# Optimization experiments

Measured on AMD Instinct MI355X. Metric: run time of the kernel, lower is better.

The kernel has to match this reference:

```python
import jax, jax.numpy as jnp
import numpy as np

ALPHA = 1.5
N_ITER = 50
N_ROWS, N_CLASSES = 4096, 32000


def tsallis_bisect(X, alpha=ALPHA, n_iter=N_ITER):
    """Entmax/Tsallis simplex projection via 50-step bisection (matches
    the standard entmax-bisect forward used by sisl/EvSoftmax)."""
    d = X.shape[-1]
    exp = 1.0 / (alpha - 1.0)          # = 2.0 for alpha = 1.5
    Xs = X * (alpha - 1.0)
    max_val = jnp.max(Xs, axis=-1, keepdims=True)            # [N,1]
    tau_lo = max_val - 1.0
    tau_hi = max_val - (1.0 / d) ** (alpha - 1.0)
    f_lo = jnp.sum(jnp.clip(Xs - tau_lo, 0.0) ** exp, axis=-1, keepdims=True) - 1.0
    dm0 = tau_hi - tau_lo

    def body(carry, _):
        tau_lo, dm, _tau_m = carry
        dm = dm * 0.5
        tau_m = tau_lo + dm                                   # [N,1]
        p_m = jnp.clip(Xs - tau_m, 0.0) ** exp                # [N,d]
        f_m = jnp.sum(p_m, axis=-1, keepdims=True) - 1.0
        mask = (f_m * f_lo) >= 0
        tau_lo = jnp.where(mask, tau_m, tau_lo)
        return (tau_lo, dm, tau_m), None

    (_, _, tau_m), _ = jax.lax.scan(body, (tau_lo, dm0, tau_lo), None, length=n_iter)
    return jnp.clip(Xs - tau_m, 0.0) ** exp                   # final p_m


def setup_inputs() -> dict:
    key = jax.random.key(0)
    X = jax.random.normal(key, (N_ROWS, N_CLASSES), dtype=jnp.float32)
    return {"X": X}


def reference(X):
    p_star = tsallis_bisect(X, ALPHA, N_ITER)
    p_star = p_star / jnp.sum(p_star, axis=1, keepdims=True)
    # safe log: value identical to log(p_star) (log(0) = -inf), but with a
    # well-defined (zero) subgradient at exactly-sparse entries.
    return jnp.where(p_star > 0, jnp.log(jnp.where(p_star > 0, p_star, 1.0)), -jnp.inf)
```

## Files before the change

kernel.cpp:

```cpp
#include <hip/hip_runtime.h>
#include <math.h>


#define NCOLS    32000
#define TPBA     512
#define NFULL    15
#define TAILBASE 30720
#define TAILTHR  320
#define NWAVE    8
#define SEGB     320
#define CAPR     (SEGB * NWAVE)
#define NSLOT    (CAPR / 64)
#define MSEG     512
#define SENT16   ((unsigned short)0xC2C0)
#define CSF      0.0055901699437494742f

__device__ __forceinline__ float wred_max(float x) {
#pragma unroll
  for (int o = 1; o < 64; o <<= 1) x = fmaxf(x, __shfl_xor(x, o, 64));
  return x;
}
__device__ __forceinline__ float wred_addf(float x) {
#pragma unroll
  for (int o = 1; o < 64; o <<= 1) x += __shfl_xor(x, o, 64);
  return x;
}
__device__ __forceinline__ unsigned short to_bf16_safe(float x) {
  unsigned int u = __float_as_uint(x);
  u += 0x7FFFu + ((u >> 16) & 1u);
  unsigned short h = (unsigned short)(u >> 16);
  if ((h & 0x7F80u) == 0x7F80u) h = SENT16;
  return h;
}

__global__ __launch_bounds__(TPBA, 4)
void tsa_stream(const float* __restrict__ X, unsigned short* __restrict__ Out,
                float* __restrict__ tauv, int* __restrict__ cnt,
                float* __restrict__ vals, unsigned short* __restrict__ idxs) {
  __shared__ float s_redf[NWAVE];
  __shared__ int   s_ovf;
  const int t    = threadIdx.x;
  const int lane = t & 63;
  const int wid  = t >> 6;
  const size_t row = blockIdx.x;
  const float* __restrict__ xr      = X + row * (size_t)NCOLS;
  unsigned short* __restrict__ orow = Out + row * (size_t)NCOLS;

  float4 v[16];
#pragma unroll
  for (int j = 0; j < NFULL; ++j)
    v[j] = *reinterpret_cast<const float4*>(xr + j * 2048 + t * 4);
  if (t < TAILTHR)
    v[15] = *reinterpret_cast<const float4*>(xr + TAILBASE + t * 4);
  else
    v[15] = make_float4(-1e30f, -1e30f, -1e30f, -1e30f);

  {
    const unsigned long long SF = 0xC2C0C2C0C2C0C2C0ull;
    unsigned long long* o8 = reinterpret_cast<unsigned long long*>(orow);
#pragma unroll
    for (int i = 0; i < 16; ++i) {
      const int p = t + i * TPBA;
      if (p < NCOLS / 4) __builtin_nontemporal_store(SF, o8 + p);
    }
  }
  if (t == 0) s_ovf = 0;

  float m = -1e30f;
#pragma unroll
  for (int j = 0; j < 16; ++j)
    m = fmaxf(m, fmaxf(fmaxf(v[j].x, v[j].y), fmaxf(v[j].z, v[j].w)));
  m = wred_max(m);
  if (lane == 0) s_redf[wid] = m;
  __syncthreads();
  float mm = s_redf[0];
#pragma unroll
  for (int w = 1; w < NWAVE; ++w) mm = fmaxf(mm, s_redf[w]);
  const float max_val = 0.5f * mm;
  const float tl0 = max_val - 1.0f;
  if (t == 0) tauv[row] = max_val;

  int myc = 0;
#pragma unroll
  for (int j = 0; j < 16; ++j) {
    myc += (v[j].x * 0.5f > tl0) + (v[j].y * 0.5f > tl0) +
           (v[j].z * 0.5f > tl0) + (v[j].w * 0.5f > tl0);
  }
  int pre = myc;
#pragma unroll
  for (int o = 1; o < 64; o <<= 1) {
    int y = __shfl_up(pre, o, 64);
    if (lane >= o) pre += y;
  }
  const int wtot = __shfl(pre, 63, 64);
  if (wtot > SEGB) {
    if (lane == 0) s_ovf = 1;
  } else {
    int wpos = pre - myc;
    float* __restrict__ vb = vals + row * (size_t)CAPR + wid * SEGB;
    unsigned short* __restrict__ ib = idxs + row * (size_t)CAPR + wid * SEGB;
#pragma unroll
    for (int j = 0; j < 16; ++j) {
      const int gidx = (j < NFULL) ? (j * 2048 + t * 4) : (TAILBASE + t * 4);
      float x;
      x = v[j].x * 0.5f; if (x > tl0) { vb[wpos] = x; ib[wpos] = (unsigned short)(gidx + 0); ++wpos; }
      x = v[j].y * 0.5f; if (x > tl0) { vb[wpos] = x; ib[wpos] = (unsigned short)(gidx + 1); ++wpos; }
      x = v[j].z * 0.5f; if (x > tl0) { vb[wpos] = x; ib[wpos] = (unsigned short)(gidx + 2); ++wpos; }
      x = v[j].w * 0.5f; if (x > tl0) { vb[wpos] = x; ib[wpos] = (unsigned short)(gidx + 3); ++wpos; }
    }
    if (lane == 63) cnt[row * NWAVE + wid] = wtot;
  }
  __syncthreads();

  if (s_ovf) {
    if (t == 0) cnt[row * NWAVE] = -1;
    const float th = max_val - CSF;
    auto bsum = [&](float tau) -> float {
      float q = 0.f;
#pragma unroll
      for (int j = 0; j < 16; ++j) {
        float r;
        r = fmaxf(v[j].x * 0.5f - tau, 0.f); q = fmaf(r, r, q);
        r = fmaxf(v[j].y * 0.5f - tau, 0.f); q = fmaf(r, r, q);
        r = fmaxf(v[j].z * 0.5f - tau, 0.f); q = fmaf(r, r, q);
        r = fmaxf(v[j].w * 0.5f - tau, 0.f); q = fmaf(r, r, q);
      }
      q = wred_addf(q);
      if (lane == 0) s_redf[wid] = q;
      __syncthreads();
      float tt = s_redf[0];
#pragma unroll
      for (int w = 1; w < NWAVE; ++w) tt += s_redf[w];
      __syncthreads();
      return tt;
    };
    float tau_lo = tl0, dmv = th - tl0, tau_m = tl0;
    const float f_lo = bsum(tau_lo) - 1.0f;
#pragma unroll 1
    for (int it = 0; it < 50; ++it) {
      dmv *= 0.5f;
      const float tm = tau_lo + dmv;
      if (tm == tau_lo) { tau_m = tau_lo; break; }
      tau_m = tm;
      const float fm = bsum(tm) - 1.0f;
      if (fm * f_lo >= 0.0f) tau_lo = tm;
    }
    const float sf = bsum(tau_m);
#pragma unroll
    for (int j = 0; j < 16; ++j) {
      const bool act = (j < NFULL) || (t < TAILTHR);
      if (act) {
        const int gidx = (j < NFULL) ? (j * 2048 + t * 4) : (TAILBASE + t * 4);
        unsigned short h[4];
        float rc, pn;
        rc = fmaxf(v[j].x * 0.5f - tau_m, 0.f); pn = (rc * rc) / sf; h[0] = (pn > 0.f) ? to_bf16_safe(logf(pn)) : SENT16;
        rc = fmaxf(v[j].y * 0.5f - tau_m, 0.f); pn = (rc * rc) / sf; h[1] = (pn > 0.f) ? to_bf16_safe(logf(pn)) : SENT16;
        rc = fmaxf(v[j].z * 0.5f - tau_m, 0.f); pn = (rc * rc) / sf; h[2] = (pn > 0.f) ? to_bf16_safe(logf(pn)) : SENT16;
        rc = fmaxf(v[j].w * 0.5f - tau_m, 0.f); pn = (rc * rc) / sf; h[3] = (pn > 0.f) ? to_bf16_safe(logf(pn)) : SENT16;
        *reinterpret_cast<uint2*>(orow + gidx) =
            make_uint2((unsigned)h[0] | ((unsigned)h[1] << 16),
                       (unsigned)h[2] | ((unsigned)h[3] << 16));
      }
    }
  }
}

__global__ __launch_bounds__(512, 4)
void tsa_bisect(unsigned short* __restrict__ Out,
                const float* __restrict__ tauv, const int* __restrict__ cnt,
                const float* __restrict__ vals,
                const unsigned short* __restrict__ idxs, int nrows) {
  const int t    = threadIdx.x;
  const int lane = t & 63;
  const int wid  = t >> 6;
  const int row  = blockIdx.x * NWAVE + wid;
  if (row >= nrows) return;

  int c8 = (lane < NWAVE) ? cnt[row * NWAVE + lane] : 0;
  const int c0 = __shfl(c8, 0, 64);
  if (c0 < 0) return;

  const float* __restrict__ vb = vals + (size_t)row * CAPR;

  float cv[NSLOT];
#pragma unroll
  for (int r = 0; r < NSLOT; ++r) cv[r] = vb[lane + r * 64];
#pragma unroll
  for (int r = 0; r < NSLOT; ++r) {
    const int cs = __shfl(c8, r / 5, 64);
    if ((r % 5) * 64 + lane >= cs) cv[r] = -1e30f;
  }

  const float max_val = tauv[row];
  const float tl0 = max_val - 1.0f;
  const float th  = max_val - CSF;

  auto fsum = [&](float tau) -> float {
    float q0 = 0.f, q1 = 0.f, q2 = 0.f, q3 = 0.f;
#pragma unroll
    for (int r = 0; r < NSLOT; r += 4) {
      float a;
      a = fmaxf(cv[r + 0] - tau, 0.f); q0 = fmaf(a, a, q0);
      a = fmaxf(cv[r + 1] - tau, 0.f); q1 = fmaf(a, a, q1);
      a = fmaxf(cv[r + 2] - tau, 0.f); q2 = fmaf(a, a, q2);
      a = fmaxf(cv[r + 3] - tau, 0.f); q3 = fmaf(a, a, q3);
    }
    return wred_addf((q0 + q1) + (q2 + q3));
  };

  float tau_lo = tl0, dmv = th - tl0, tau_m = tl0;
  const float f_lo = fsum(tau_lo) - 1.0f;
#pragma unroll 1
  for (int it = 0; it < 50; ++it) {
    dmv *= 0.5f;
    const float tm = tau_lo + dmv;
    if (tm == tau_lo) { tau_m = tau_lo; break; }
    tau_m = tm;
    const float fm = fsum(tm) - 1.0f;
    if (fm * f_lo >= 0.0f) tau_lo = tm;
  }
  const float sf = fsum(tau_m);

  unsigned short* __restrict__ orow = Out + (size_t)row * NCOLS;
  const unsigned short* __restrict__ ib = idxs + (size_t)row * CAPR;
#pragma unroll 1
  for (int r = 0; r < NSLOT; ++r) {
    const float rc = fmaxf(cv[r] - tau_m, 0.f);
    const float pn = (rc * rc) / sf;
    if (pn > 0.f) orow[ib[lane + r * 64]] = to_bf16_safe(logf(pn));
  }
}

__global__ __launch_bounds__(TPBA, 8)
void tsa_mono(const float* __restrict__ X, unsigned short* __restrict__ Out) {
  __shared__ float          s_redf[NWAVE];
  __shared__ int            s_segk[NWAVE];
  __shared__ int            s_ovf;
  __shared__ float          s_tau, s_sf;
  __shared__ float          s_cand[MSEG * NWAVE];
  __shared__ unsigned short s_cidx[MSEG * NWAVE];

  const int t = threadIdx.x, lane = t & 63, wid = t >> 6;
  const size_t row = blockIdx.x;
  const float* __restrict__ xr      = X + row * (size_t)NCOLS;
  unsigned short* __restrict__ orow = Out + row * (size_t)NCOLS;

  float m = -1e30f;
#pragma unroll 5
  for (int j = 0; j < NFULL; ++j) {
    float4 a = *reinterpret_cast<const float4*>(xr + j * 2048 + t * 4);
    m = fmaxf(m, fmaxf(fmaxf(a.x, a.y), fmaxf(a.z, a.w)));
  }
  if (t < TAILTHR) {
    float4 a = *reinterpret_cast<const float4*>(xr + TAILBASE + t * 4);
    m = fmaxf(m, fmaxf(fmaxf(a.x, a.y), fmaxf(a.z, a.w)));
  }
  m = wred_max(m);
  if (lane == 0) s_redf[wid] = m;
  if (t == 0) s_ovf = 0;
  __syncthreads();
  float mm = s_redf[0];
#pragma unroll
  for (int w = 1; w < NWAVE; ++w) mm = fmaxf(mm, s_redf[w]);
  const float max_val = 0.5f * mm;
  const float tau_lo0 = max_val - 1.0f;
  const float tau_hi  = max_val - CSF;

  {
    int base = 0;
    const int seg0 = wid * MSEG;
    const unsigned long long SFILL = 0xC2C0C2C0C2C0C2C0ull;
#pragma unroll 2
    for (int j = 0; j <= NFULL; ++j) {
      const bool act = (j < NFULL) || (t < TAILTHR);
      const int gidx = (j < NFULL) ? (j * 2048 + t * 4) : (TAILBASE + t * 4);
      float x0 = -1e30f, x1 = -1e30f, x2 = -1e30f, x3 = -1e30f;
      if (act) {
        float4 a = *reinterpret_cast<const float4*>(xr + gidx);
        x0 = a.x * 0.5f; x1 = a.y * 0.5f; x2 = a.z * 0.5f; x3 = a.w * 0.5f;
        __builtin_nontemporal_store(
            SFILL, reinterpret_cast<unsigned long long*>(orow + gidx));
      }
      int c = (x0 > tau_lo0) + (x1 > tau_lo0) + (x2 > tau_lo0) + (x3 > tau_lo0);
      int pre = c;
#pragma unroll
      for (int o = 1; o < 64; o <<= 1) {
        int y = __shfl_up(pre, o, 64);
        if (lane >= o) pre += y;
      }
      const int tot = __shfl(pre, 63, 64);
      if (base + tot <= MSEG) {
        int pos = seg0 + base + (pre - c);
        if (x0 > tau_lo0) { s_cand[pos] = x0; s_cidx[pos] = (unsigned short)(gidx + 0); ++pos; }
        if (x1 > tau_lo0) { s_cand[pos] = x1; s_cidx[pos] = (unsigned short)(gidx + 1); ++pos; }
        if (x2 > tau_lo0) { s_cand[pos] = x2; s_cidx[pos] = (unsigned short)(gidx + 2); ++pos; }
        if (x3 > tau_lo0) { s_cand[pos] = x3; s_cidx[pos] = (unsigned short)(gidx + 3); ++pos; }
      } else if (lane == 0) {
        s_ovf = 1;
      }
      base += tot;
    }
    if (base <= MSEG) {
      const int kp = (base + 63) & ~63;
      for (int i = base + lane; i < kp; i += 64) s_cand[seg0 + i] = -1e30f;
    }
    if (lane == 0) s_segk[wid] = base;
  }
  __syncthreads();

  if (s_ovf == 0) {
    if (wid == 0) {
      int kp[NWAVE];
#pragma unroll
      for (int s = 0; s < NWAVE; ++s) kp[s] = (s_segk[s] + 63) & ~63;
      auto fsum = [&](float tau) -> float {
        float q = 0.f;
#pragma unroll 1
        for (int s = 0; s < NWAVE; ++s) {
          const float* cs = s_cand + s * MSEG;
          const int kps = kp[s];
          for (int i = lane; i < kps; i += 64) {
            const float r = fmaxf(cs[i] - tau, 0.f);
            q = fmaf(r, r, q);
          }
        }
        return wred_addf(q);
      };
      float tau_lo = tau_lo0, dmv = tau_hi - tau_lo0, tau_m = tau_lo0;
      const float f_lo = fsum(tau_lo) - 1.0f;
#pragma unroll 1
      for (int it = 0; it < 50; ++it) {
        dmv *= 0.5f;
        const float tm = tau_lo + dmv;
        if (tm == tau_lo) { tau_m = tau_lo; break; }
        tau_m = tm;
        const float fm = fsum(tm) - 1.0f;
        if (fm * f_lo >= 0.0f) tau_lo = tm;
      }
      const float sf = fsum(tau_m);
      if (lane == 0) { s_tau = tau_m; s_sf = sf; }
    }
    __syncthreads();
    const float tau_m = s_tau, sf = s_sf;
#pragma unroll 1
    for (int s = 0; s < NWAVE; ++s) {
      const int ks = s_segk[s];
      for (int i = t; i < ks; i += TPBA) {
        const float rc = fmaxf(s_cand[s * MSEG + i] - tau_m, 0.f);
        const float pn = (rc * rc) / sf;
        if (pn > 0.f) orow[s_cidx[s * MSEG + i]] = to_bf16_safe(logf(pn));
      }
    }
  } else {
    auto bsum = [&](float tau) -> float {
      float q = 0.f;
#pragma unroll 4
      for (int j = 0; j <= NFULL; ++j) {
        const bool act = (j < NFULL) || (t < TAILTHR);
        const int gidx = (j < NFULL) ? (j * 2048 + t * 4) : (TAILBASE + t * 4);
        if (act) {
          float4 a = *reinterpret_cast<const float4*>(xr + gidx);
          float r;
          r = fmaxf(a.x * 0.5f - tau, 0.f); q = fmaf(r, r, q);
          r = fmaxf(a.y * 0.5f - tau, 0.f); q = fmaf(r, r, q);
          r = fmaxf(a.z * 0.5f - tau, 0.f); q = fmaf(r, r, q);
          r = fmaxf(a.w * 0.5f - tau, 0.f); q = fmaf(r, r, q);
        }
      }
      q = wred_addf(q);
      if (lane == 0) s_redf[wid] = q;
      __syncthreads();
      float tot = s_redf[0];
#pragma unroll
      for (int w = 1; w < NWAVE; ++w) tot += s_redf[w];
      __syncthreads();
      return tot;
    };
    float tau_lo = tau_lo0, dmv = tau_hi - tau_lo0, tau_m = tau_lo0;
    const float f_lo = bsum(tau_lo) - 1.0f;
#pragma unroll 1
    for (int it = 0; it < 50; ++it) {
      dmv *= 0.5f;
      const float tm = tau_lo + dmv;
      if (tm == tau_lo) { tau_m = tau_lo; break; }
      tau_m = tm;
      const float fm = bsum(tm) - 1.0f;
      if (fm * f_lo >= 0.0f) tau_lo = tm;
    }
    const float sf = bsum(tau_m);
#pragma unroll 1
    for (int j = 0; j <= NFULL; ++j) {
      const bool act = (j < NFULL) || (t < TAILTHR);
      const int gidx = (j < NFULL) ? (j * 2048 + t * 4) : (TAILBASE + t * 4);
      if (act) {
        float4 a = *reinterpret_cast<const float4*>(xr + gidx);
        unsigned short h[4];
        float rc, pn;
        rc = fmaxf(a.x * 0.5f - tau_m, 0.f); pn = (rc * rc) / sf; h[0] = (pn > 0.f) ? to_bf16_safe(logf(pn)) : SENT16;
        rc = fmaxf(a.y * 0.5f - tau_m, 0.f); pn = (rc * rc) / sf; h[1] = (pn > 0.f) ? to_bf16_safe(logf(pn)) : SENT16;
        rc = fmaxf(a.z * 0.5f - tau_m, 0.f); pn = (rc * rc) / sf; h[2] = (pn > 0.f) ? to_bf16_safe(logf(pn)) : SENT16;
        rc = fmaxf(a.w * 0.5f - tau_m, 0.f); pn = (rc * rc) / sf; h[3] = (pn > 0.f) ? to_bf16_safe(logf(pn)) : SENT16;
        *reinterpret_cast<uint2*>(orow + gidx) =
            make_uint2((unsigned)h[0] | ((unsigned)h[1] << 16),
                       (unsigned)h[2] | ((unsigned)h[3] << 16));
      }
    }
  }
}

extern "C" void kernel_launch(void* const* d_in, const int* in_sizes, int n_in,
                              void* d_out, int out_size, void* d_ws, size_t ws_size,
                              hipStream_t stream) {
  const float* X = (const float*)d_in[0];
  unsigned short* Out = (unsigned short*)d_out;
  const int rows = in_sizes[0] / NCOLS;

  const size_t offT = 0;
  const size_t offC = (size_t)rows * 4;
  const size_t offV = (offC + (size_t)rows * NWAVE * 4 + 255) & ~(size_t)255;
  const size_t offI = (offV + (size_t)rows * CAPR * 4 + 255) & ~(size_t)255;
  const size_t need = offI + (size_t)rows * CAPR * 2;

  if (ws_size >= need) {
    char* ws = (char*)d_ws;
    float* tauv = (float*)(ws + offT);
    int* cnt = (int*)(ws + offC);
    float* vals = (float*)(ws + offV);
    unsigned short* idxs = (unsigned short*)(ws + offI);
    hipLaunchKernelGGL(tsa_stream, dim3(rows), dim3(TPBA), 0, stream,
                       X, Out, tauv, cnt, vals, idxs);
    const int gridB = (rows + NWAVE - 1) / NWAVE;
    hipLaunchKernelGGL(tsa_bisect, dim3(gridB), dim3(512), 0, stream,
                       Out, tauv, cnt, vals, idxs, rows);
  } else {
    hipLaunchKernelGGL(tsa_mono, dim3(rows), dim3(TPBA), 0, stream, X, Out);
  }
}
```

Measured before the change: 215.2 us.

## Use ballot-based candidate compaction and move -inf fill into bisect kernel

In the streaming kernel, the per-thread count, prefix scan and sequential candidate writes are replaced by per-component wave ballots with mbcnt lane prefixes. Candidate stores are now interleaved across lanes and coalesced, and overflow is detected incrementally. The sentinel fill of each output row moves out of the streaming kernel into the per-row bisect wave, using 16-byte stores followed by an explicit vmcnt wait before the scatter. This lightens the streaming kernel's write traffic, but the bulk fill now runs in the smaller bisect grid. Rows that take the overflow path no longer get the pre-fill, so the fallback code may need to write the full row.

```diff
diff --git a/kernel.cpp b/kernel.cpp
--- a/kernel.cpp
+++ b/kernel.cpp
@@ -25,6 +25,10 @@
   for (int o = 1; o < 64; o <<= 1) x += __shfl_xor(x, o, 64);
   return x;
 }
+__device__ __forceinline__ int lane_prefix(unsigned long long m) {
+  return __builtin_amdgcn_mbcnt_hi((unsigned)(m >> 32),
+         __builtin_amdgcn_mbcnt_lo((unsigned)m, 0));
+}
 __device__ __forceinline__ unsigned short to_bf16_safe(float x) {
   unsigned int u = __float_as_uint(x);
   u += 0x7FFFu + ((u >> 16) & 1u);
@@ -54,16 +58,6 @@
     v[15] = *reinterpret_cast<const float4*>(xr + TAILBASE + t * 4);
   else
     v[15] = make_float4(-1e30f, -1e30f, -1e30f, -1e30f);
-
-  {
-    const unsigned long long SF = 0xC2C0C2C0C2C0C2C0ull;
-    unsigned long long* o8 = reinterpret_cast<unsigned long long*>(orow);
-#pragma unroll
-    for (int i = 0; i < 16; ++i) {
-      const int p = t + i * TPBA;
-      if (p < NCOLS / 4) __builtin_nontemporal_store(SF, o8 + p);
-    }
-  }
   if (t == 0) s_ovf = 0;
 
   float m = -1e30f;
@@ -80,35 +74,33 @@
   const float tl0 = max_val - 1.0f;
   if (t == 0) tauv[row] = max_val;
 
-  int myc = 0;
-#pragma unroll
-  for (int j = 0; j < 16; ++j) {
-    myc += (v[j].x * 0.5f > tl0) + (v[j].y * 0.5f > tl0) +
-           (v[j].z * 0.5f > tl0) + (v[j].w * 0.5f > tl0);
-  }
-  int pre = myc;
-#pragma unroll
-  for (int o = 1; o < 64; o <<= 1) {
-    int y = __shfl_up(pre, o, 64);
-    if (lane >= o) pre += y;
-  }
-  const int wtot = __shfl(pre, 63, 64);
-  if (wtot > SEGB) {
-    if (lane == 0) s_ovf = 1;
-  } else {
-    int wpos = pre - myc;
+  {
+    int base = 0;
     float* __restrict__ vb = vals + row * (size_t)CAPR + wid * SEGB;
     unsigned short* __restrict__ ib = idxs + row * (size_t)CAPR + wid * SEGB;
 #pragma unroll
     for (int j = 0; j < 16; ++j) {
       const int gidx = (j < NFULL) ? (j * 2048 + t * 4) : (TAILBASE + t * 4);
-      float x;
-      x = v[j].x * 0.5f; if (x > tl0) { vb[wpos] = x; ib[wpos] = (unsigned short)(gidx + 0); ++wpos; }
-      x = v[j].y * 0.5f; if (x > tl0) { vb[wpos] = x; ib[wpos] = (unsigned short)(gidx + 1); ++wpos; }
-      x = v[j].z * 0.5f; if (x > tl0) { vb[wpos] = x; ib[wpos] = (unsigned short)(gidx + 2); ++wpos; }
-      x = v[j].w * 0.5f; if (x > tl0) { vb[wpos] = x; ib[wpos] = (unsigned short)(gidx + 3); ++wpos; }
-    }
-    if (lane == 63) cnt[row * NWAVE + wid] = wtot;
+      const float xs[4] = {v[j].x * 0.5f, v[j].y * 0.5f,
+                           v[j].z * 0.5f, v[j].w * 0.5f};
+#pragma unroll
+      for (int c = 0; c < 4; ++c) {
+        const bool b = xs[c] > tl0;
+        const unsigned long long mk = __ballot(b);
+        const int tot = __popcll(mk);
+        if (base + tot <= SEGB) {
+          if (b) {
+            const int pos = base + lane_prefix(mk);
+            vb[pos] = xs[c];
+            ib[pos] = (unsigned short)(gidx + c);
+          }
+        } else if (lane == 0) {
+          s_ovf = 1;
+        }
+        base += tot;
+      }
+    }
+    if (base <= SEGB && lane == 0) cnt[row * NWAVE + wid] = base;
   }
   __syncthreads();
 
@@ -180,8 +172,20 @@
   const int c0 = __shfl(c8, 0, 64);
   if (c0 < 0) return;
 
+  unsigned short* __restrict__ orow = Out + (size_t)row * NCOLS;
+
+  {
+    const unsigned int sp = 0xC2C0C2C0u;
+    const uint4 fillv = make_uint4(sp, sp, sp, sp);
+    uint4* o4 = reinterpret_cast<uint4*>(orow);
+#pragma unroll 1
+    for (int r = 0; r < 63; ++r) {
+      const int p = lane + r * 64;
+      if (p < NCOLS / 8) o4[p] = fillv;
+    }
+  }
+
   const float* __restrict__ vb = vals + (size_t)row * CAPR;
-
   float cv[NSLOT];
 #pragma unroll
   for (int r = 0; r < NSLOT; ++r) cv[r] = vb[lane + r * 64];
@@ -221,7 +225,8 @@
   }
   const float sf = fsum(tau_m);
 
-  unsigned short* __restrict__ orow = Out + (size_t)row * NCOLS;
+  asm volatile("s_waitcnt vmcnt(0)" ::: "memory");
+
   const unsigned short* __restrict__ ib = idxs + (size_t)row * CAPR;
 #pragma unroll 1
   for (int r = 0; r < NSLOT; ++r) {
```

Measured after the change: 243.0 us. 12.9% more time.
